# Optimization experiments

Measured on AMD Instinct MI355X. Metric: run time of the kernel, lower is better.

## Reference

```python
import jax, jax.numpy as jnp
import numpy as np

EPS = 1e-6  # kernel_epsilon
NUM_HEADS = 16
NUM_SCALES = 3
ROPE_BASE = 10000.0


def _rope(x, base=ROPE_BASE):
    # x: [B, S, N, D]; rotary applied along seq dim 1 (RotaryPositionEmbedding.forward)
    B, S, N, D = x.shape
    inv_freq = 1.0 / (base ** (jnp.arange(0, D, 2, dtype=jnp.float32) / D))  # [D/2]
    t = jnp.arange(S, dtype=jnp.float32)
    freqs = t[:, None] * inv_freq[None, :]            # [S, D/2]
    emb = jnp.concatenate([freqs, freqs], axis=-1)    # [S, D]
    cos = jnp.cos(emb)[None, :, None, :]
    sin = jnp.sin(emb)[None, :, None, :]
    x1, x2 = jnp.split(x, 2, axis=-1)
    rot = jnp.concatenate([-x2, x1], axis=-1)         # rotate_half
    return x * cos + rot * sin


def _kernel(x):
    # elu kernel: F.elu(x) + 1.0 + epsilon
    return jax.nn.elu(x) + 1.0 + EPS


def setup_inputs() -> dict:
    key = jax.random.key(0)
    ks = jax.random.split(key, 12)
    B, S, H = 4, 2048, 1024
    sc = 1.0 / np.sqrt(H)
    inp = {
        "hidden_states": jax.random.normal(ks[0], (B, S, H), dtype=jnp.float32),
        "attention_mask": jnp.ones((B, S), dtype=jnp.float32),
        "Wq": jax.random.normal(ks[1], (H, H), dtype=jnp.float32) * sc,
        "bq": jnp.zeros((H,), dtype=jnp.float32),
        "Wk": jax.random.normal(ks[2], (H, H), dtype=jnp.float32) * sc,
        "bk": jnp.zeros((H,), dtype=jnp.float32),
        "Wv": jax.random.normal(ks[3], (H, H), dtype=jnp.float32) * sc,
        "bv": jnp.zeros((H,), dtype=jnp.float32),
        "Wo": jax.random.normal(ks[4], (H, H), dtype=jnp.float32) * sc,
        "bo": jnp.zeros((H,), dtype=jnp.float32),
        "Wg": jax.random.normal(ks[5], (H, 1), dtype=jnp.float32) * sc,
        "bg": jnp.zeros((1,), dtype=jnp.float32),  # gate_init_bias = 0.0
        "decay_factors": jnp.ones((NUM_SCALES,), dtype=jnp.float32) * 0.9,
        "gate_weights": jnp.ones((NUM_SCALES,), dtype=jnp.float32) / NUM_SCALES,
    }
    return inp


def reference(hidden_states, attention_mask, Wq, bq, Wk, bk, Wv, bv, Wo, bo,
              Wg, bg, decay_factors, gate_weights):
    B, S, H = hidden_states.shape
    N = NUM_HEADS
    D = H // N
    scaling = D ** -0.5

    q = (hidden_states @ Wq + bq).reshape(B, S, N, D)
    k = (hidden_states @ Wk + bk).reshape(B, S, N, D)
    v = (hidden_states @ Wv + bv).reshape(B, S, N, D)

    # rotary position embeddings on q, k
    q = _rope(q)
    k = _rope(k)

    # kernel feature maps (elu + 1 + eps), query scaling
    q = _kernel(q) * scaling
    k = _kernel(k)

    # apply padding mask to keys/values (mask.unsqueeze(-1).unsqueeze(-1))
    m = attention_mask[:, :, None, None]
    k = k * m
    v = v * m

    # linear (kernelized) attention over the sequence, fused form of
    # einsum('bsnk,bsnv->bsnkv').sum(dim=1)
    kv = jnp.einsum('bsnk,bsnv->bnkv', k, v)          # [B, N, D, D]
    k_sum = jnp.sum(k, axis=1)                        # [B, N, D]
    num = jnp.einsum('bsnk,bnkv->bsnv', q, kv)        # [B, S, N, D]
    den = jnp.einsum('bsnk,bnk->bsn', q, k_sum) + EPS
    attn_out = num / den[..., None]                   # [B, S, N, D]

    # multi-scale memory: starts at zero, one decayed update with this chunk
    decay_sig = jax.nn.sigmoid(decay_factors)                  # [M]
    memory = (1.0 - decay_sig)[None, :, None, None, None] * kv[:, None]  # [B,M,N,D,D]
    mem_scaled = jnp.einsum('bsnk,bmnkv->bmsnv', q, memory)    # [B,M,S,N,D]
    gate_soft = jax.nn.softmax(gate_weights, axis=0)           # [M]
    mem_out = jnp.sum(mem_scaled * gate_soft[None, :, None, None, None], axis=1)

    # sigmoid gate blending local linear attention with memory readout
    g = jax.nn.sigmoid(hidden_states @ Wg + bg)[..., None]     # [B, S, 1, 1]
    combined = g * attn_out + (1.0 - g) * mem_out              # [B, S, N, D]

    out = combined.reshape(B, S, H) @ Wo + bo
    return out
```

## Files before the change

### kernel.cpp

```cpp
#include <hip/hip_runtime.h>
#include <math.h>

#define B_   4
#define S_   2048
#define H_   1024
#define NH   16
#define HD   64
#define T_   (B_ * S_)
#define NCH  16

typedef unsigned short u16;
typedef __bf16 bf16x8 __attribute__((ext_vector_type(8)));
typedef float  f32x4  __attribute__((ext_vector_type(4)));

__device__ __forceinline__ float elu_k(float x) {
    return (x > 0.f ? x : (expf(x) - 1.f)) + 1.000001f;
}

__device__ __forceinline__ u16 f2bf(float x) {
    union { float f; unsigned int u; } v; v.f = x;
    unsigned int r = v.u + 0x7FFFu + ((v.u >> 16) & 1u);
    return (u16)(r >> 16);
}

__device__ __forceinline__ float bfl(unsigned int u) {
    union { unsigned int u; float f; } v; v.u = u << 16; return v.f;
}
__device__ __forceinline__ float bfh(unsigned int u) {
    union { unsigned int u; float f; } v; v.u = u & 0xFFFF0000u; return v.f;
}

__device__ __forceinline__ void async_load16(const u16* g, u16* l) {
    __builtin_amdgcn_global_load_lds(
        (const __attribute__((address_space(1))) void*)g,
        (__attribute__((address_space(3))) void*)l,
        16, 0, 0);
}

__global__ void coeff_kernel(const float* __restrict__ decay,
                             const float* __restrict__ gate,
                             float* __restrict__ coeff) {
    if (threadIdx.x == 0 && blockIdx.x == 0) {
        float g0 = gate[0], g1 = gate[1], g2 = gate[2];
        float mx = fmaxf(g0, fmaxf(g1, g2));
        float e0 = expf(g0 - mx), e1 = expf(g1 - mx), e2 = expf(g2 - mx);
        float inv = 1.f / (e0 + e1 + e2);
        float es[3] = {e0, e1, e2};
        float c = 0.f;
        for (int m = 0; m < 3; m++) {
            float ds = 1.f / (1.f + expf(-decay[m]));
            c += es[m] * inv * (1.f - ds);
        }
        *coeff = c;
    }
}

__global__ void rope_table_kernel(float* __restrict__ cosT,
                                  float* __restrict__ sinT) {
    int idx = blockIdx.x * blockDim.x + threadIdx.x;
    if (idx >= S_ * 32) return;
    int s = idx >> 5, i = idx & 31;
    float inv = powf(10000.f, -(2.f * (float)i) / 64.f);
    float f = (float)s * inv;
    cosT[idx] = cosf(f);
    sinT[idx] = sinf(f);
}

__global__ __launch_bounds__(256) void cvt_bf16_kernel(
    const float* __restrict__ in, u16* __restrict__ out, int n4) {
    int i = blockIdx.x * 256 + threadIdx.x;
    if (i >= n4) return;
    float4 f = ((const float4*)in)[i];
    ushort4 u;
    u.x = f2bf(f.x); u.y = f2bf(f.y); u.z = f2bf(f.z); u.w = f2bf(f.w);
    ((ushort4*)out)[i] = u;
}

__global__ __launch_bounds__(256) void pack_w_kernel(
    const float* __restrict__ Wq, const float* __restrict__ Wk,
    const float* __restrict__ Wv, const float* __restrict__ Wo,
    u16* __restrict__ Wt) {
    __shared__ u16 tile[64][65];
    const float* W = (blockIdx.z == 0) ? Wq :
                     (blockIdx.z == 1) ? Wk :
                     (blockIdx.z == 2) ? Wv : Wo;
    int nt = blockIdx.x * 64, kt = blockIdx.y * 64;
    int tid = threadIdx.x;
#pragma unroll
    for (int it = 0; it < 16; it++) {
        int i = it * 256 + tid;
        int kr = i >> 6, nc = i & 63;
        tile[kr][nc] = f2bf(W[(size_t)(kt + kr) * H_ + nt + nc]);
    }
    __syncthreads();
    size_t wbase = (size_t)blockIdx.z * H_;
#pragma unroll
    for (int it = 0; it < 16; it++) {
        int i = it * 256 + tid;
        int nr = i >> 6, kc = i & 63;
        Wt[(wbase + nt + nr) * H_ + kt + kc] = tile[kc][nr];
    }
}

__global__ void pack_bias_kernel(const float* __restrict__ bq,
                                 const float* __restrict__ bk,
                                 const float* __restrict__ bv,
                                 float* __restrict__ bqkv) {
    int i = blockIdx.x * 256 + threadIdx.x;
    if (i >= 3072) return;
    bqkv[i] = (i < 1024) ? bq[i] : (i < 2048) ? bk[i - 1024] : bv[i - 2048];
}

__global__ __launch_bounds__(256) void gemm_qkv_kernel(
    const u16* __restrict__ A, const u16* __restrict__ Bt,
    const float* __restrict__ bias, const float* __restrict__ mask,
    const float* __restrict__ cosT, const float* __restrict__ sinT,
    u16* __restrict__ qb, u16* __restrict__ kb, u16* __restrict__ vb) {
    constexpr int K = 1024;
    __shared__ u16 Asl[128 * 32];
    __shared__ u16 Bsl[128 * 32];
    const int tid  = threadIdx.x;
    const int wave = tid >> 6, lane = tid & 63;
    const int wm = (wave & 1) * 64, wn = (wave >> 1) * 64;
    const int bm = blockIdx.y * 128, bn = blockIdx.x * 128;
    const int l15 = lane & 15, quad = lane >> 4;

    f32x4 acc[4][4];
#pragma unroll
    for (int i = 0; i < 4; i++)
#pragma unroll
        for (int j = 0; j < 4; j++) acc[i][j] = {0.f, 0.f, 0.f, 0.f};

    for (int k0 = 0; k0 < K; k0 += 32) {
#pragma unroll
        for (int r = 0; r < 2; r++) {
            int i = r * 256 + wave * 64 + lane;
            async_load16(&A[(size_t)(bm + (i >> 2)) * K + k0 + (i & 3) * 8],
                         &Asl[(r * 256 + wave * 64) * 8]);
        }
#pragma unroll
        for (int r = 0; r < 2; r++) {
            int i = r * 256 + wave * 64 + lane;
            async_load16(&Bt[(size_t)(bn + (i >> 2)) * K + k0 + (i & 3) * 8],
                         &Bsl[(r * 256 + wave * 64) * 8]);
        }
        asm volatile("s_waitcnt vmcnt(0)" ::: "memory");
        __syncthreads();

        bf16x8 af[4], bfr[4];
#pragma unroll
        for (int mi = 0; mi < 4; mi++)
            af[mi] = *(const bf16x8*)&Asl[(wm + mi * 16 + l15) * 32 + quad * 8];
#pragma unroll
        for (int nj = 0; nj < 4; nj++)
            bfr[nj] = *(const bf16x8*)&Bsl[(wn + nj * 16 + l15) * 32 + quad * 8];
#pragma unroll
        for (int mi = 0; mi < 4; mi++)
#pragma unroll
            for (int nj = 0; nj < 4; nj++)
                acc[mi][nj] = __builtin_amdgcn_mfma_f32_16x16x32_bf16(
                    af[mi], bfr[nj], acc[mi][nj], 0, 0, 0);
        __syncthreads();
    }

    const int colbase = bn + wn;
    const int region  = colbase >> 10;
    const int n       = (colbase & 1023) >> 6;
    float bc[4];
#pragma unroll
    for (int nj = 0; nj < 4; nj++) bc[nj] = bias[colbase + nj * 16 + l15];
    u16* outp = (region == 0) ? qb : (region == 1) ? kb : vb;

#pragma unroll
    for (int mi = 0; mi < 4; mi++) {
#pragma unroll
        for (int r = 0; r < 4; r++) {
            int row = bm + wm + mi * 16 + quad * 4 + r;
            int b = row >> 11, s = row & (S_ - 1);
            size_t obase = ((size_t)(b * 16 + n) * S_ + s) * 64;
            if (region < 2) {
                float mfac = (region == 0) ? 0.125f : mask[row];
#pragma unroll
                for (int p = 0; p < 2; p++) {
                    int d1 = p * 16 + l15;
                    float c  = cosT[s * 32 + d1];
                    float sn = sinT[s * 32 + d1];
                    float x1 = acc[mi][p][r]     + bc[p];
                    float x2 = acc[mi][p + 2][r] + bc[p + 2];
                    float r1 = x1 * c - x2 * sn;
                    float r2 = x2 * c + x1 * sn;
                    outp[obase + d1]      = f2bf(elu_k(r1) * mfac);
                    outp[obase + d1 + 32] = f2bf(elu_k(r2) * mfac);
                }
            } else {
                float mfac = mask[row];
#pragma unroll
                for (int nj = 0; nj < 4; nj++)
                    outp[obase + nj * 16 + l15] =
                        f2bf((acc[mi][nj][r] + bc[nj]) * mfac);
            }
        }
    }
}

__global__ __launch_bounds__(256) void gemm_bf16_kernel(
    const u16* __restrict__ A, const u16* __restrict__ Bt,
    const float* __restrict__ bias, float* __restrict__ C, int N) {
    constexpr int K = 1024;
    __shared__ u16 Asl[128 * 32];
    __shared__ u16 Bsl[128 * 32];
    const int tid  = threadIdx.x;
    const int wave = tid >> 6, lane = tid & 63;
    const int wm = (wave & 1) * 64, wn = (wave >> 1) * 64;
    const int bm = blockIdx.y * 128, bn = blockIdx.x * 128;
    const int l15 = lane & 15, quad = lane >> 4;

    f32x4 acc[4][4];
#pragma unroll
    for (int i = 0; i < 4; i++)
#pragma unroll
        for (int j = 0; j < 4; j++) acc[i][j] = {0.f, 0.f, 0.f, 0.f};

    for (int k0 = 0; k0 < K; k0 += 32) {
#pragma unroll
        for (int r = 0; r < 2; r++) {
            int i = r * 256 + wave * 64 + lane;
            async_load16(&A[(size_t)(bm + (i >> 2)) * K + k0 + (i & 3) * 8],
                         &Asl[(r * 256 + wave * 64) * 8]);
        }
#pragma unroll
        for (int r = 0; r < 2; r++) {
            int i = r * 256 + wave * 64 + lane;
            async_load16(&Bt[(size_t)(bn + (i >> 2)) * K + k0 + (i & 3) * 8],
                         &Bsl[(r * 256 + wave * 64) * 8]);
        }
        asm volatile("s_waitcnt vmcnt(0)" ::: "memory");
        __syncthreads();

        bf16x8 af[4], bfr[4];
#pragma unroll
        for (int mi = 0; mi < 4; mi++)
            af[mi] = *(const bf16x8*)&Asl[(wm + mi * 16 + l15) * 32 + quad * 8];
#pragma unroll
        for (int nj = 0; nj < 4; nj++)
            bfr[nj] = *(const bf16x8*)&Bsl[(wn + nj * 16 + l15) * 32 + quad * 8];
#pragma unroll
        for (int mi = 0; mi < 4; mi++)
#pragma unroll
            for (int nj = 0; nj < 4; nj++)
                acc[mi][nj] = __builtin_amdgcn_mfma_f32_16x16x32_bf16(
                    af[mi], bfr[nj], acc[mi][nj], 0, 0, 0);
        __syncthreads();
    }

#pragma unroll
    for (int mi = 0; mi < 4; mi++) {
#pragma unroll
        for (int nj = 0; nj < 4; nj++) {
            int col = bn + wn + nj * 16 + l15;
            float bcol = bias[col];
#pragma unroll
            for (int r = 0; r < 4; r++) {
                int row = bm + wm + mi * 16 + quad * 4 + r;
                C[(size_t)row * N + col] = acc[mi][nj][r] + bcol;
            }
        }
    }
}

__global__ __launch_bounds__(256) void gate_kernel(
    const float* __restrict__ hs, const float* __restrict__ Wg,
    const float* __restrict__ bg, float* __restrict__ g) {
    int w = (blockIdx.x * 256 + threadIdx.x) >> 6;
    int lane = threadIdx.x & 63;
    const float* row = hs + (size_t)w * H_;
    float s = 0.f;
    for (int i = lane; i < H_; i += 64) s = fmaf(row[i], Wg[i], s);
#pragma unroll
    for (int off = 32; off > 0; off >>= 1) s += __shfl_down(s, off);
    if (lane == 0) g[w] = 1.f / (1.f + expf(-(s + bg[0])));
}

__global__ __launch_bounds__(256) void kv_part_kernel(
    const u16* __restrict__ kb, const u16* __restrict__ vb,
    float* __restrict__ kvpart, float* __restrict__ kspart) {
    int bn = blockIdx.x;
    const int rows = S_ / NCH;
    int s0 = blockIdx.y * rows;
    int tid = threadIdx.x;
    int ti = tid >> 4, tj = tid & 15;
    __shared__ float ks[16][64], vs[16][64];
    float acc[4][4] = {};
    float ksacc = 0.f;
    const u16* kbase = kb + (size_t)bn * (S_ * 64) + (size_t)s0 * 64;
    const u16* vbase = vb + (size_t)bn * (S_ * 64) + (size_t)s0 * 64;
    for (int ss = 0; ss < rows; ss += 16) {
        {
            int half = tid >> 7;
            int c = tid & 127;
            int rr = c >> 3, col = (c & 7) * 8;
            const u16* src = (half ? vbase : kbase) + (size_t)(ss + rr) * 64 + col;
            uint4 raw = *(const uint4*)src;
            float* dst = half ? &vs[rr][col] : &ks[rr][col];
            dst[0] = bfl(raw.x); dst[1] = bfh(raw.x);
            dst[2] = bfl(raw.y); dst[3] = bfh(raw.y);
            dst[4] = bfl(raw.z); dst[5] = bfh(raw.z);
            dst[6] = bfl(raw.w); dst[7] = bfh(raw.w);
        }
        __syncthreads();
#pragma unroll
        for (int r = 0; r < 16; r++) {
            float a[4], bb[4];
#pragma unroll
            for (int i = 0; i < 4; i++) a[i] = ks[r][ti * 4 + i];
#pragma unroll
            for (int j = 0; j < 4; j++) bb[j] = vs[r][tj * 4 + j];
#pragma unroll
            for (int i = 0; i < 4; i++)
#pragma unroll
                for (int j = 0; j < 4; j++)
                    acc[i][j] = fmaf(a[i], bb[j], acc[i][j]);
        }
        if (tid < 64) {
#pragma unroll
            for (int r = 0; r < 16; r++) ksacc += ks[r][tid];
        }
        __syncthreads();
    }
    size_t obase = ((size_t)blockIdx.y * 64 + bn) * 4096;
#pragma unroll
    for (int i = 0; i < 4; i++)
#pragma unroll
        for (int j = 0; j < 4; j++)
            kvpart[obase + (size_t)(ti * 4 + i) * 64 + tj * 4 + j] = acc[i][j];
    if (tid < 64)
        kspart[((size_t)blockIdx.y * 64 + bn) * 64 + tid] = ksacc;
}

__global__ __launch_bounds__(256) void reduce_part_kernel(
    const float* __restrict__ part, float* __restrict__ out,
    int n, int stride) {
    int i = blockIdx.x * 256 + threadIdx.x;
    if (i >= n) return;
    float s = 0.f;
#pragma unroll
    for (int c = 0; c < NCH; c++) s += part[(size_t)c * stride + i];
    out[i] = s;
}

__global__ __launch_bounds__(256) void combine_kernel(
    const u16* __restrict__ qb, const float* __restrict__ kvb,
    const float* __restrict__ ksum, const float* __restrict__ g,
    const float* __restrict__ coeffp, u16* __restrict__ cmb) {
    int bn = blockIdx.x;
    int b = bn >> 4, n = bn & 15;
    __shared__ u16 qs[256 * 72];
    __shared__ u16 kvT[64 * 72];
    __shared__ u16 ksl[128];
    int tid = threadIdx.x;
    int s0 = blockIdx.y * 256;

    const u16* qsrc = qb + (size_t)bn * (S_ * 64) + (size_t)s0 * 64;
    for (int c = tid; c < 2048; c += 256) {
        int t = c >> 3, k8 = (c & 7) * 8;
        float4 tmp = *(const float4*)(qsrc + (size_t)c * 8);
        *(float4*)&qs[t * 72 + k8] = tmp;
    }
    for (int c = tid; c < 1024; c += 256) {
        int i = c >> 4, d4 = (c & 15) * 4;
        float4 kvv = *(const float4*)&kvb[(size_t)bn * 4096 + i * 64 + d4];
        kvT[(d4 + 0) * 72 + i] = f2bf(kvv.x);
        kvT[(d4 + 1) * 72 + i] = f2bf(kvv.y);
        kvT[(d4 + 2) * 72 + i] = f2bf(kvv.z);
        kvT[(d4 + 3) * 72 + i] = f2bf(kvv.w);
    }
    if (tid < 64)        ksl[tid] = f2bf(ksum[bn * 64 + tid]);
    else if (tid < 128)  ksl[tid] = 0;
    __syncthreads();

    int wave = tid >> 6, lane = tid & 63;
    int l15 = lane & 15, quad = lane >> 4;
    int wt = wave * 64;

    int ko0 = (l15 == 0) ? quad * 8      : 64;
    int ko1 = (l15 == 0) ? 32 + quad * 8 : 64;
    bf16x8 ksf0 = *(const bf16x8*)&ksl[ko0 & ~0u];
    bf16x8 ksf1 = *(const bf16x8*)&ksl[ko1];

    bf16x8 bfr0[4], bfr1[4];
#pragma unroll
    for (int nj = 0; nj < 4; nj++) {
        bfr0[nj] = *(const bf16x8*)&kvT[(nj * 16 + l15) * 72 + quad * 8];
        bfr1[nj] = *(const bf16x8*)&kvT[(nj * 16 + l15) * 72 + 32 + quad * 8];
    }

    f32x4 acc[4][4], dacc[4];
#pragma unroll
    for (int i = 0; i < 4; i++) {
        dacc[i] = {0.f, 0.f, 0.f, 0.f};
#pragma unroll
        for (int j = 0; j < 4; j++) acc[i][j] = {0.f, 0.f, 0.f, 0.f};
    }

#pragma unroll
    for (int mi = 0; mi < 4; mi++) {
        bf16x8 a0 = *(const bf16x8*)&qs[(wt + mi * 16 + l15) * 72 + quad * 8];
        bf16x8 a1 = *(const bf16x8*)&qs[(wt + mi * 16 + l15) * 72 + 32 + quad * 8];
        dacc[mi] = __builtin_amdgcn_mfma_f32_16x16x32_bf16(a0, ksf0, dacc[mi], 0, 0, 0);
        dacc[mi] = __builtin_amdgcn_mfma_f32_16x16x32_bf16(a1, ksf1, dacc[mi], 0, 0, 0);
#pragma unroll
        for (int nj = 0; nj < 4; nj++) {
            acc[mi][nj] = __builtin_amdgcn_mfma_f32_16x16x32_bf16(
                a0, bfr0[nj], acc[mi][nj], 0, 0, 0);
            acc[mi][nj] = __builtin_amdgcn_mfma_f32_16x16x32_bf16(
                a1, bfr1[nj], acc[mi][nj], 0, 0, 0);
        }
    }

    float coeff = *coeffp;
#pragma unroll
    for (int mi = 0; mi < 4; mi++) {
#pragma unroll
        for (int r = 0; r < 4; r++) {
            int s = s0 + wt + mi * 16 + quad * 4 + r;
            int t = b * S_ + s;
            float den = __shfl(dacc[mi][r], lane & 48) + 1e-6f;
            float gv = g[t];
            float w1 = gv / den + (1.f - gv) * coeff;
#pragma unroll
            for (int nj = 0; nj < 4; nj++) {
                int d = nj * 16 + l15;
                cmb[(size_t)t * H_ + n * 64 + d] = f2bf(acc[mi][nj][r] * w1);
            }
        }
    }
}

extern "C" void kernel_launch(void* const* d_in, const int* in_sizes, int n_in,
                              void* d_out, int out_size, void* d_ws, size_t ws_size,
                              hipStream_t stream) {
    const float* hs    = (const float*)d_in[0];
    const float* mask  = (const float*)d_in[1];
    const float* Wq    = (const float*)d_in[2];
    const float* bq    = (const float*)d_in[3];
    const float* Wk    = (const float*)d_in[4];
    const float* bk    = (const float*)d_in[5];
    const float* Wv    = (const float*)d_in[6];
    const float* bv    = (const float*)d_in[7];
    const float* Wo    = (const float*)d_in[8];
    const float* bo    = (const float*)d_in[9];
    const float* Wg    = (const float*)d_in[10];
    const float* bg    = (const float*)d_in[11];
    const float* decay = (const float*)d_in[12];
    const float* gate  = (const float*)d_in[13];
    float* out = (float*)d_out;

    float* ws     = (float*)d_ws;
    float* kvb    = ws;
    float* ksum   = kvb + 262144;
    float* gbuf   = ksum + 4096;
    float* coeff  = gbuf + 8192;
    float* cosT   = coeff + 64;
    float* sinT   = cosT + 65536;
    float* bqkv   = sinT + 65536;
    float* kspart = bqkv + 4096;
    float* kvpart = kspart + 65536;
    u16*   hsb    = (u16*)(kvpart + 4194304);
    u16*   Wt     = hsb + (size_t)T_ * H_;
    u16*   WoT    = Wt + (size_t)3072 * H_;
    u16*   qb     = Wt + (size_t)4096 * H_;
    u16*   kb     = qb + (size_t)T_ * H_;
    u16*   vb     = kb + (size_t)T_ * H_;
    u16*   cmb    = vb + (size_t)T_ * H_;

    coeff_kernel<<<1, 64, 0, stream>>>(decay, gate, coeff);
    rope_table_kernel<<<(S_ * 32 + 255) / 256, 256, 0, stream>>>(cosT, sinT);
    cvt_bf16_kernel<<<(T_ * H_ / 4 + 255) / 256, 256, 0, stream>>>(
        hs, hsb, T_ * H_ / 4);
    pack_w_kernel<<<dim3(16, 16, 4), 256, 0, stream>>>(Wq, Wk, Wv, Wo, Wt);
    pack_bias_kernel<<<12, 256, 0, stream>>>(bq, bk, bv, bqkv);

    gemm_qkv_kernel<<<dim3(3072 / 128, T_ / 128), 256, 0, stream>>>(
        hsb, Wt, bqkv, mask, cosT, sinT, qb, kb, vb);

    gate_kernel<<<T_ / 4, 256, 0, stream>>>(hs, Wg, bg, gbuf);

    kv_part_kernel<<<dim3(B_ * NH, NCH), 256, 0, stream>>>(
        kb, vb, kvpart, kspart);
    reduce_part_kernel<<<(262144 + 255) / 256, 256, 0, stream>>>(
        kvpart, kvb, 262144, 262144);
    reduce_part_kernel<<<(4096 + 255) / 256, 256, 0, stream>>>(
        kspart, ksum, 4096, 4096);

    combine_kernel<<<dim3(B_ * NH, S_ / 256), 256, 0, stream>>>(
        qb, kvb, ksum, gbuf, coeff, cmb);

    gemm_bf16_kernel<<<dim3(H_ / 128, T_ / 128), 256, 0, stream>>>(
        cmb, WoT, bo, out, H_);
}
```

Before: 288.7 us.

## Fuse small prep kernels, merge gate into bf16 cast, deepen GEMM K-step

```diff
diff --git a/kernel.cpp b/kernel.cpp
--- a/kernel.cpp
+++ b/kernel.cpp
@@ -37,10 +37,23 @@
         16, 0, 0);
 }
 
-__global__ void coeff_kernel(const float* __restrict__ decay,
-                             const float* __restrict__ gate,
-                             float* __restrict__ coeff) {
-    if (threadIdx.x == 0 && blockIdx.x == 0) {
+__global__ __launch_bounds__(256) void prep_kernel(
+    const float* __restrict__ decay, const float* __restrict__ gate,
+    float* __restrict__ coeff, float* __restrict__ cosT,
+    float* __restrict__ sinT, const float* __restrict__ bq,
+    const float* __restrict__ bk, const float* __restrict__ bv,
+    float* __restrict__ bqkv) {
+    int idx = blockIdx.x * 256 + threadIdx.x;
+    if (idx < S_ * 32) {
+        int s = idx >> 5, i = idx & 31;
+        float inv = powf(10000.f, -(2.f * (float)i) / 64.f);
+        float f = (float)s * inv;
+        cosT[idx] = cosf(f);
+        sinT[idx] = sinf(f);
+    } else if (idx < S_ * 32 + 3072) {
+        int i = idx - S_ * 32;
+        bqkv[i] = (i < 1024) ? bq[i] : (i < 2048) ? bk[i - 1024] : bv[i - 2048];
+    } else if (idx == S_ * 32 + 3072) {
         float g0 = gate[0], g1 = gate[1], g2 = gate[2];
         float mx = fmaxf(g0, fmaxf(g1, g2));
         float e0 = expf(g0 - mx), e1 = expf(g1 - mx), e2 = expf(g2 - mx);
@@ -55,25 +68,27 @@
     }
 }
 
-__global__ void rope_table_kernel(float* __restrict__ cosT,
-                                  float* __restrict__ sinT) {
-    int idx = blockIdx.x * blockDim.x + threadIdx.x;
-    if (idx >= S_ * 32) return;
-    int s = idx >> 5, i = idx & 31;
-    float inv = powf(10000.f, -(2.f * (float)i) / 64.f);
-    float f = (float)s * inv;
-    cosT[idx] = cosf(f);
-    sinT[idx] = sinf(f);
-}
-
-__global__ __launch_bounds__(256) void cvt_bf16_kernel(
-    const float* __restrict__ in, u16* __restrict__ out, int n4) {
-    int i = blockIdx.x * 256 + threadIdx.x;
-    if (i >= n4) return;
-    float4 f = ((const float4*)in)[i];
+__global__ __launch_bounds__(256) void cvt_gate_kernel(
+    const float* __restrict__ hs, const float* __restrict__ Wg,
+    const float* __restrict__ bg, u16* __restrict__ hsb,
+    float* __restrict__ gbuf) {
+    int t = blockIdx.x;
+    int i = threadIdx.x;
+    float4 f = ((const float4*)(hs + (size_t)t * H_))[i];
+    float4 w = ((const float4*)Wg)[i];
     ushort4 u;
     u.x = f2bf(f.x); u.y = f2bf(f.y); u.z = f2bf(f.z); u.w = f2bf(f.w);
-    ((ushort4*)out)[i] = u;
+    ((ushort4*)(hsb + (size_t)t * H_))[i] = u;
+    float s = f.x * w.x + f.y * w.y + f.z * w.z + f.w * w.w;
+#pragma unroll
+    for (int off = 32; off > 0; off >>= 1) s += __shfl_down(s, off);
+    __shared__ float wsum[4];
+    if ((i & 63) == 0) wsum[i >> 6] = s;
+    __syncthreads();
+    if (i == 0) {
+        float tot = wsum[0] + wsum[1] + wsum[2] + wsum[3];
+        gbuf[t] = 1.f / (1.f + expf(-(tot + bg[0])));
+    }
 }
 
 __global__ __launch_bounds__(256) void pack_w_kernel(
@@ -102,14 +117,40 @@
     }
 }
 
-__global__ void pack_bias_kernel(const float* __restrict__ bq,
-                                 const float* __restrict__ bk,
-                                 const float* __restrict__ bv,
-                                 float* __restrict__ bqkv) {
-    int i = blockIdx.x * 256 + threadIdx.x;
-    if (i >= 3072) return;
-    bqkv[i] = (i < 1024) ? bq[i] : (i < 2048) ? bk[i - 1024] : bv[i - 2048];
-}
+#define GEMM_KLOOP(A_, Bt_, bm_, bn_)                                         \
+    for (int k0 = 0; k0 < K; k0 += 64) {                                      \
+        _Pragma("unroll")                                                     \
+        for (int h = 0; h < 2; h++) {                                         \
+            _Pragma("unroll")                                                 \
+            for (int i = 0; i < 2; i++) {                                     \
+                int r0 = (wave * 2 + i) * 16;                                 \
+                int rr = lane >> 2, cc = lane & 3;                            \
+                async_load16(&A_[(size_t)(bm_ + r0 + rr) * K + k0 + h * 32 + cc * 8], \
+                             &Asl[h][r0 * 32]);                               \
+                async_load16(&Bt_[(size_t)(bn_ + r0 + rr) * K + k0 + h * 32 + cc * 8], \
+                             &Bsl[h][r0 * 32]);                               \
+            }                                                                 \
+        }                                                                     \
+        asm volatile("s_waitcnt vmcnt(0)" ::: "memory");                      \
+        __syncthreads();                                                      \
+        _Pragma("unroll")                                                     \
+        for (int h = 0; h < 2; h++) {                                         \
+            bf16x8 af[4], bfr[4];                                             \
+            _Pragma("unroll")                                                 \
+            for (int mi = 0; mi < 4; mi++)                                    \
+                af[mi] = *(const bf16x8*)&Asl[h][(wm + mi * 16 + l15) * 32 + quad * 8]; \
+            _Pragma("unroll")                                                 \
+            for (int nj = 0; nj < 4; nj++)                                    \
+                bfr[nj] = *(const bf16x8*)&Bsl[h][(wn + nj * 16 + l15) * 32 + quad * 8]; \
+            _Pragma("unroll")                                                 \
+            for (int mi = 0; mi < 4; mi++)                                    \
+                _Pragma("unroll")                                             \
+                for (int nj = 0; nj < 4; nj++)                                \
+                    acc[mi][nj] = __builtin_amdgcn_mfma_f32_16x16x32_bf16(    \
+                        af[mi], bfr[nj], acc[mi][nj], 0, 0, 0);               \
+        }                                                                     \
+        __syncthreads();                                                      \
+    }
 
 __global__ __launch_bounds__(256) void gemm_qkv_kernel(
     const u16* __restrict__ A, const u16* __restrict__ Bt,
@@ -117,8 +158,8 @@
     const float* __restrict__ cosT, const float* __restrict__ sinT,
     u16* __restrict__ qb, u16* __restrict__ kb, u16* __restrict__ vb) {
     constexpr int K = 1024;
-    __shared__ u16 Asl[128 * 32];
-    __shared__ u16 Bsl[128 * 32];
+    __shared__ u16 Asl[2][128 * 32];
+    __shared__ u16 Bsl[2][128 * 32];
     const int tid  = threadIdx.x;
     const int wave = tid >> 6, lane = tid & 63;
     const int wm = (wave & 1) * 64, wn = (wave >> 1) * 64;
@@ -131,37 +172,7 @@
 #pragma unroll
         for (int j = 0; j < 4; j++) acc[i][j] = {0.f, 0.f, 0.f, 0.f};
 
-    for (int k0 = 0; k0 < K; k0 += 32) {
-#pragma unroll
-        for (int r = 0; r < 2; r++) {
-            int i = r * 256 + wave * 64 + lane;
-            async_load16(&A[(size_t)(bm + (i >> 2)) * K + k0 + (i & 3) * 8],
-                         &Asl[(r * 256 + wave * 64) * 8]);
-        }
-#pragma unroll
-        for (int r = 0; r < 2; r++) {
-            int i = r * 256 + wave * 64 + lane;
-            async_load16(&Bt[(size_t)(bn + (i >> 2)) * K + k0 + (i & 3) * 8],
-                         &Bsl[(r * 256 + wave * 64) * 8]);
-        }
-        asm volatile("s_waitcnt vmcnt(0)" ::: "memory");
-        __syncthreads();
-
-        bf16x8 af[4], bfr[4];
-#pragma unroll
-        for (int mi = 0; mi < 4; mi++)
-            af[mi] = *(const bf16x8*)&Asl[(wm + mi * 16 + l15) * 32 + quad * 8];
-#pragma unroll
-        for (int nj = 0; nj < 4; nj++)
-            bfr[nj] = *(const bf16x8*)&Bsl[(wn + nj * 16 + l15) * 32 + quad * 8];
-#pragma unroll
-        for (int mi = 0; mi < 4; mi++)
-#pragma unroll
-            for (int nj = 0; nj < 4; nj++)
-                acc[mi][nj] = __builtin_amdgcn_mfma_f32_16x16x32_bf16(
-                    af[mi], bfr[nj], acc[mi][nj], 0, 0, 0);
-        __syncthreads();
-    }
+    GEMM_KLOOP(A, Bt, bm, bn)
 
     const int colbase = bn + wn;
     const int region  = colbase >> 10;
@@ -203,12 +214,12 @@
     }
 }
 
-__global__ __launch_bounds__(256) void gemm_bf16_kernel(
+__global__ __launch_bounds__(256) void gemm_out_kernel(
     const u16* __restrict__ A, const u16* __restrict__ Bt,
     const float* __restrict__ bias, float* __restrict__ C, int N) {
     constexpr int K = 1024;
-    __shared__ u16 Asl[128 * 32];
-    __shared__ u16 Bsl[128 * 32];
+    __shared__ u16 Asl[2][128 * 32];
+    __shared__ u16 Bsl[2][128 * 32];
     const int tid  = threadIdx.x;
     const int wave = tid >> 6, lane = tid & 63;
     const int wm = (wave & 1) * 64, wn = (wave >> 1) * 64;
@@ -221,37 +232,7 @@
 #pragma unroll
         for (int j = 0; j < 4; j++) acc[i][j] = {0.f, 0.f, 0.f, 0.f};
 
-    for (int k0 = 0; k0 < K; k0 += 32) {
-#pragma unroll
-        for (int r = 0; r < 2; r++) {
-            int i = r * 256 + wave * 64 + lane;
-            async_load16(&A[(size_t)(bm + (i >> 2)) * K + k0 + (i & 3) * 8],
-                         &Asl[(r * 256 + wave * 64) * 8]);
-        }
-#pragma unroll
-        for (int r = 0; r < 2; r++) {
-            int i = r * 256 + wave * 64 + lane;
-            async_load16(&Bt[(size_t)(bn + (i >> 2)) * K + k0 + (i & 3) * 8],
-                         &Bsl[(r * 256 + wave * 64) * 8]);
-        }
-        asm volatile("s_waitcnt vmcnt(0)" ::: "memory");
-        __syncthreads();
-
-        bf16x8 af[4], bfr[4];
-#pragma unroll
-        for (int mi = 0; mi < 4; mi++)
-            af[mi] = *(const bf16x8*)&Asl[(wm + mi * 16 + l15) * 32 + quad * 8];
-#pragma unroll
-        for (int nj = 0; nj < 4; nj++)
-            bfr[nj] = *(const bf16x8*)&Bsl[(wn + nj * 16 + l15) * 32 + quad * 8];
-#pragma unroll
-        for (int mi = 0; mi < 4; mi++)
-#pragma unroll
-            for (int nj = 0; nj < 4; nj++)
-                acc[mi][nj] = __builtin_amdgcn_mfma_f32_16x16x32_bf16(
-                    af[mi], bfr[nj], acc[mi][nj], 0, 0, 0);
-        __syncthreads();
-    }
+    GEMM_KLOOP(A, Bt, bm, bn)
 
 #pragma unroll
     for (int mi = 0; mi < 4; mi++) {
@@ -266,19 +247,6 @@
             }
         }
     }
-}
-
-__global__ __launch_bounds__(256) void gate_kernel(
-    const float* __restrict__ hs, const float* __restrict__ Wg,
-    const float* __restrict__ bg, float* __restrict__ g) {
-    int w = (blockIdx.x * 256 + threadIdx.x) >> 6;
-    int lane = threadIdx.x & 63;
-    const float* row = hs + (size_t)w * H_;
-    float s = 0.f;
-    for (int i = lane; i < H_; i += 64) s = fmaf(row[i], Wg[i], s);
-#pragma unroll
-    for (int off = 32; off > 0; off >>= 1) s += __shfl_down(s, off);
-    if (lane == 0) g[w] = 1.f / (1.f + expf(-(s + bg[0])));
 }
 
 __global__ __launch_bounds__(256) void kv_part_kernel(
@@ -338,14 +306,21 @@
 }
 
 __global__ __launch_bounds__(256) void reduce_part_kernel(
-    const float* __restrict__ part, float* __restrict__ out,
-    int n, int stride) {
+    const float* __restrict__ kvpart, const float* __restrict__ kspart,
+    float* __restrict__ kvb, float* __restrict__ ksum) {
     int i = blockIdx.x * 256 + threadIdx.x;
-    if (i >= n) return;
-    float s = 0.f;
-#pragma unroll
-    for (int c = 0; c < NCH; c++) s += part[(size_t)c * stride + i];
-    out[i] = s;
+    if (i < 262144) {
+        float s = 0.f;
+#pragma unroll
+        for (int c = 0; c < NCH; c++) s += kvpart[(size_t)c * 262144 + i];
+        kvb[i] = s;
+    } else if (i < 262144 + 4096) {
+        int j = i - 262144;
+        float s = 0.f;
+#pragma unroll
+        for (int c = 0; c < NCH; c++) s += kspart[(size_t)c * 4096 + j];
+        ksum[j] = s;
+    }
 }
 
 __global__ __launch_bounds__(256) void combine_kernel(
@@ -384,7 +359,7 @@
 
     int ko0 = (l15 == 0) ? quad * 8      : 64;
     int ko1 = (l15 == 0) ? 32 + quad * 8 : 64;
-    bf16x8 ksf0 = *(const bf16x8*)&ksl[ko0 & ~0u];
+    bf16x8 ksf0 = *(const bf16x8*)&ksl[ko0];
     bf16x8 ksf1 = *(const bf16x8*)&ksl[ko1];
 
     bf16x8 bfr0[4], bfr1[4];
@@ -473,28 +448,22 @@
     u16*   vb     = kb + (size_t)T_ * H_;
     u16*   cmb    = vb + (size_t)T_ * H_;
 
-    coeff_kernel<<<1, 64, 0, stream>>>(decay, gate, coeff);
-    rope_table_kernel<<<(S_ * 32 + 255) / 256, 256, 0, stream>>>(cosT, sinT);
-    cvt_bf16_kernel<<<(T_ * H_ / 4 + 255) / 256, 256, 0, stream>>>(
-        hs, hsb, T_ * H_ / 4);
+    prep_kernel<<<(S_ * 32 + 3072 + 256) / 256 + 1, 256, 0, stream>>>(
+        decay, gate, coeff, cosT, sinT, bq, bk, bv, bqkv);
+    cvt_gate_kernel<<<T_, 256, 0, stream>>>(hs, Wg, bg, hsb, gbuf);
     pack_w_kernel<<<dim3(16, 16, 4), 256, 0, stream>>>(Wq, Wk, Wv, Wo, Wt);
-    pack_bias_kernel<<<12, 256, 0, stream>>>(bq, bk, bv, bqkv);
 
     gemm_qkv_kernel<<<dim3(3072 / 128, T_ / 128), 256, 0, stream>>>(
         hsb, Wt, bqkv, mask, cosT, sinT, qb, kb, vb);
 
-    gate_kernel<<<T_ / 4, 256, 0, stream>>>(hs, Wg, bg, gbuf);
-
     kv_part_kernel<<<dim3(B_ * NH, NCH), 256, 0, stream>>>(
         kb, vb, kvpart, kspart);
-    reduce_part_kernel<<<(262144 + 255) / 256, 256, 0, stream>>>(
-        kvpart, kvb, 262144, 262144);
-    reduce_part_kernel<<<(4096 + 255) / 256, 256, 0, stream>>>(
-        kspart, ksum, 4096, 4096);
+    reduce_part_kernel<<<(262144 + 4096 + 255) / 256, 256, 0, stream>>>(
+        kvpart, kspart, kvb, ksum);
 
     combine_kernel<<<dim3(B_ * NH, S_ / 256), 256, 0, stream>>>(
         qb, kvb, ksum, gbuf, coeff, cmb);
 
-    gemm_bf16_kernel<<<dim3(H_ / 128, T_ / 128), 256, 0, stream>>>(
+    gemm_out_kernel<<<dim3(H_ / 128, T_ / 128), 256, 0, stream>>>(
         cmb, WoT, bo, out, H_);
 }
```

Result: faster. 272.5 us (-5.6%).
